# Performance work log

Hardware: AMD Instinct MI355X
Metric: run time of the kernel (lower is better)

Reference implementation:

```python
import jax, jax.numpy as jnp
import numpy as np

NUM_NODES = 2048
NUM_OPS = 8
D, F, K = 64, 64, 64
H_NG = 128
H_EE = 64


def _make_edges(n):
    # edges[0]=i (src), edges[1]=j (dst) for i in [2,n), j in [0,i)
    src = np.concatenate([np.full(i, i, dtype=np.int64) for i in range(2, n)])
    dst = np.concatenate([np.arange(i, dtype=np.int64) for i in range(2, n)])
    return np.stack([src, dst])


def setup_inputs() -> dict:
    key = jax.random.key(0)
    ks = jax.random.split(key, 8)
    n = NUM_NODES
    s = lambda k, shape, fan_in: jax.random.normal(k, shape, jnp.float32) * (1.0 / np.sqrt(fan_in))
    return {
        "embed": jax.random.normal(ks[0], (n, D), jnp.float32),
        "W1": s(ks[1], (D, H_NG), D), "b1": jnp.zeros((H_NG,), jnp.float32),
        "W2": s(ks[2], (H_NG, H_NG), H_NG), "b2": jnp.zeros((H_NG,), jnp.float32),
        "W3": s(ks[3], (H_NG, F), H_NG), "b3": jnp.zeros((F,), jnp.float32),
        "We1": s(ks[4], (2 * F, H_EE), 2 * F), "be1": jnp.zeros((H_EE,), jnp.float32),
        "We2": s(ks[5], (H_EE, K), H_EE), "be2": jnp.zeros((K,), jnp.float32),
        "Wop": s(ks[6], (K, NUM_OPS), K), "bop": jnp.zeros((NUM_OPS,), jnp.float32),
        "edges": jnp.asarray(_make_edges(n)),
        "weights": jnp.ones((_make_edges(n).shape[1],), jnp.float32),
    }


def gcn_conv(x, W, b, src, dst, ew, n):
    # PyG GCNConv: x' = D^{-1/2} (A + I) D^{-1/2} (x W) + b, aggregated at dst
    h = x @ W
    loop = jnp.arange(n)
    src2 = jnp.concatenate([src, loop])
    dst2 = jnp.concatenate([dst, loop])
    w2 = jnp.concatenate([ew, jnp.ones((n,), x.dtype)])
    deg = jax.ops.segment_sum(w2, dst2, num_segments=n)
    dinv = jnp.where(deg > 0, jax.lax.rsqrt(deg), 0.0)
    norm = dinv[src2] * w2 * dinv[dst2]
    out = jax.ops.segment_sum(h[src2] * norm[:, None], dst2, num_segments=n)
    return out + b


def reference(embed, W1, b1, W2, b2, W3, b3, We1, be1, We2, be2, Wop, bop, edges, weights):
    n = embed.shape[0]
    src, dst = edges[0], edges[1]
    h = jax.nn.relu(gcn_conv(embed, W1, b1, src, dst, weights, n))
    h = jax.nn.relu(gcn_conv(h, W2, b2, src, dst, weights, n))
    h = jax.nn.relu(gcn_conv(h, W3, b3, src, dst, weights, n))  # [n, F]
    e = jnp.concatenate([h[src], h[dst]], axis=-1)              # [E, 2F]
    e = jax.nn.relu(e @ We1 + be1)
    e = jax.nn.relu(e @ We2 + be2)
    o = e @ Wop + bop                                            # [E, num_ops]
    p = jax.nn.softmax(o, axis=-1)
    # forward loop skips i == num_nodes-1; those rows of p remain zero
    mask = (src < n - 1)[:, None]
    return jnp.where(mask, p, 0.0)
```

## Files before the change

### kernel.cpp

```cpp
#include <hip/hip_runtime.h>
#include <math.h>

#define NN 2048
#define LASTN 2047

typedef __attribute__((ext_vector_type(8))) short short8;
typedef __attribute__((ext_vector_type(4))) float f32x4;

__device__ __forceinline__ float node_dinv(int j) {
  int deg = (j < 2) ? 2047 : (2048 - j);
  return rsqrtf((float)deg);
}

__device__ __forceinline__ void split_bf(float x, short& h, short& l) {
  unsigned u = __float_as_uint(x);
  unsigned r = u + 0x7FFFu + ((u >> 16) & 1u);
  h = (short)(r >> 16);
  float fh = __uint_as_float((r >> 16) << 16);
  float res = x - fh;
  unsigned u2 = __float_as_uint(res);
  unsigned r2 = u2 + 0x7FFFu + ((u2 >> 16) & 1u);
  l = (short)(r2 >> 16);
}

__global__ __launch_bounds__(256) void gemm_node(const float* __restrict__ X,
                                                 const float* __restrict__ W,
                                                 const float* __restrict__ bias,
                                                 float* __restrict__ C, int K, int N) {
  int idx = blockIdx.x * 256 + threadIdx.x;
  int r = idx / N;
  int c = idx - r * N;
  float a0 = 0.f, a1 = 0.f, a2 = 0.f, a3 = 0.f;
  for (int k = 0; k < K; k += 4) {
    a0 = fmaf(X[r * K + k + 0], W[(k + 0) * N + c], a0);
    a1 = fmaf(X[r * K + k + 1], W[(k + 1) * N + c], a1);
    a2 = fmaf(X[r * K + k + 2], W[(k + 2) * N + c], a2);
    a3 = fmaf(X[r * K + k + 3], W[(k + 3) * N + c], a3);
  }
  C[idx] = (a0 + a1) + (a2 + a3) + (bias ? bias[c] : 0.f);
}

__global__ __launch_bounds__(256) void gemm_ab(const float* __restrict__ X,
                                               const float* __restrict__ We1,
                                               const float* __restrict__ be1,
                                               float* __restrict__ A,
                                               float* __restrict__ B) {
  int idx = blockIdx.x * 256 + threadIdx.x;
  int r = idx >> 6, c = idx & 63;
  const float* WA = We1;
  const float* WB = We1 + 64 * 64;
  float a0 = 0.f, a1 = 0.f, b0 = 0.f, b1 = 0.f;
  for (int k = 0; k < 64; k += 2) {
    float x0 = X[r * 64 + k], x1 = X[r * 64 + k + 1];
    a0 = fmaf(x0, WA[k * 64 + c], a0);
    a1 = fmaf(x1, WA[(k + 1) * 64 + c], a1);
    b0 = fmaf(x0, WB[k * 64 + c], b0);
    b1 = fmaf(x1, WB[(k + 1) * 64 + c], b1);
  }
  A[idx] = a0 + a1 + be1[c];
  B[idx] = b0 + b1;
}

__global__ __launch_bounds__(256) void gcn_agg(const float* __restrict__ H,
                                               const float* __restrict__ b,
                                               float* __restrict__ out, int N) {
  const int c = blockIdx.x;
  const int t = threadIdx.x;
  __shared__ float part[256];
  float s[8], hv[8];
  #pragma unroll
  for (int k = 0; k < 8; ++k) {
    int i = t * 8 + k;
    hv[k] = H[(size_t)i * N + c];
    s[k] = hv[k] * node_dinv(i);
  }
  float p = 0.f;
  #pragma unroll
  for (int k = 0; k < 8; ++k) p += s[k];
  part[t] = p;
  __syncthreads();
  for (int off = 1; off < 256; off <<= 1) {
    float v = part[t] + ((t + off < 256) ? part[t + off] : 0.f);
    __syncthreads();
    part[t] = v;
    __syncthreads();
  }
  float Q = (t < 255) ? part[t + 1] : 0.f;
  float Te[8];
  float acc = Q;
  #pragma unroll
  for (int k = 7; k >= 0; --k) { Te[k] = acc; acc += s[k]; }
  const float bc = b[c];
  #pragma unroll
  for (int k = 0; k < 8; ++k) {
    int j = t * 8 + k;
    float aggv = (j == 0) ? Te[1] : Te[k];
    float dj = node_dinv(j);
    float v = dj * aggv + hv[k] * dj * dj + bc;
    out[(size_t)j * N + c] = fmaxf(v, 0.f);
  }
}

__global__ __launch_bounds__(256) void prep_bfrag(const float* __restrict__ We2,
                                                  short* __restrict__ BfH,
                                                  short* __restrict__ BfL) {
  int t = blockIdx.x * 256 + threadIdx.x;
  if (t >= 512) return;
  int lane = t & 63;
  int rest = t >> 6;
  int ks = rest & 1;
  int ct = rest >> 1;
  int q = lane >> 4, l4 = lane & 15;
  int f = ct * 16 + l4;
  #pragma unroll
  for (int j = 0; j < 8; ++j) {
    int k = ks * 32 + q * 8 + j;
    float w = We2[k * 64 + f];
    short h, l;
    split_bf(w, h, l);
    int o = ((ct * 2 + ks) * 64 + lane) * 8 + j;
    BfH[o] = h;
    BfL[o] = l;
  }
}

#define CHUNK 192
#define LSTR 196

__global__ __launch_bounds__(256, 3) void edge_mlp(const float* __restrict__ Amat,
                                                   const float* __restrict__ Bmat,
                                                   const short* __restrict__ BfH,
                                                   const short* __restrict__ BfL,
                                                   const float* __restrict__ be2,
                                                   const float* __restrict__ Wop,
                                                   const float* __restrict__ bop,
                                                   float* __restrict__ out) {
  const int i = LASTN - blockIdx.x;
  const long base = (long)i * (i - 1) / 2 - 1;
  const int tid = threadIdx.x;

  if (i == LASTN) {
    const float4 z = make_float4(0.f, 0.f, 0.f, 0.f);
    for (int j = blockIdx.y * 256 + tid; j < LASTN; j += gridDim.y * 256) {
      size_t off = ((size_t)(base + j)) * 8;
      *(float4*)(out + off) = z;
      *(float4*)(out + off + 4) = z;
    }
    return;
  }

  __shared__ __align__(16) float sm[64 * LSTR];

  const int l = tid & 63, w = tid >> 6;
  const int l4 = l & 15, q = l >> 4;

  const float4* Arow = (const float4*)(Amat + (size_t)i * 64);
  const float4 a00 = Arow[q * 2], a01 = Arow[q * 2 + 1];
  const float4 a10 = Arow[8 + q * 2], a11 = Arow[8 + q * 2 + 1];

  short8 Bh[8], Bl[8];
  #pragma unroll
  for (int u = 0; u < 8; ++u) {
    Bh[u] = *(const short8*)(BfH + (u * 64 + l) * 8);
    Bl[u] = *(const short8*)(BfL + (u * 64 + l) * 8);
  }

  #pragma unroll 1
  for (int cidx = blockIdx.y; cidx * CHUNK < i; cidx += gridDim.y) {
    const int j0 = cidx * CHUNK;

    #pragma unroll 1
    for (int mt = 0; mt < 3; ++mt) {
      const int mbase = (w * 3 + mt) * 16;
      int j = j0 + mbase + l4;
      int jc = min(j, i - 1);
      const float4* Brow = (const float4*)(Bmat + (size_t)jc * 64);

      short8 ah[2], al[2];
      #pragma unroll
      for (int ks = 0; ks < 2; ++ks) {
        float4 bb0 = Brow[ks * 8 + q * 2];
        float4 bb1 = Brow[ks * 8 + q * 2 + 1];
        float4 aa0 = ks ? a10 : a00;
        float4 aa1 = ks ? a11 : a01;
        float v0 = fmaxf(aa0.x + bb0.x, 0.f), v1 = fmaxf(aa0.y + bb0.y, 0.f);
        float v2 = fmaxf(aa0.z + bb0.z, 0.f), v3 = fmaxf(aa0.w + bb0.w, 0.f);
        float v4 = fmaxf(aa1.x + bb1.x, 0.f), v5 = fmaxf(aa1.y + bb1.y, 0.f);
        float v6 = fmaxf(aa1.z + bb1.z, 0.f), v7 = fmaxf(aa1.w + bb1.w, 0.f);
        short h0, h1, h2, h3, h4, h5, h6, h7, L0, L1, L2, L3, L4, L5, L6, L7;
        split_bf(v0, h0, L0); split_bf(v1, h1, L1);
        split_bf(v2, h2, L2); split_bf(v3, h3, L3);
        split_bf(v4, h4, L4); split_bf(v5, h5, L5);
        split_bf(v6, h6, L6); split_bf(v7, h7, L7);
        ah[ks] = (short8){h0, h1, h2, h3, h4, h5, h6, h7};
        al[ks] = (short8){L0, L1, L2, L3, L4, L5, L6, L7};
      }

      f32x4 acc[4];
      #pragma unroll
      for (int ct = 0; ct < 4; ++ct) acc[ct] = (f32x4){0.f, 0.f, 0.f, 0.f};
      #pragma unroll
      for (int ct = 0; ct < 4; ++ct)
        acc[ct] = __builtin_amdgcn_mfma_f32_16x16x32_bf16(ah[0], Bh[ct * 2 + 0], acc[ct], 0, 0, 0);
      #pragma unroll
      for (int ct = 0; ct < 4; ++ct)
        acc[ct] = __builtin_amdgcn_mfma_f32_16x16x32_bf16(ah[1], Bh[ct * 2 + 1], acc[ct], 0, 0, 0);
      #pragma unroll
      for (int ct = 0; ct < 4; ++ct)
        acc[ct] = __builtin_amdgcn_mfma_f32_16x16x32_bf16(ah[0], Bl[ct * 2 + 0], acc[ct], 0, 0, 0);
      #pragma unroll
      for (int ct = 0; ct < 4; ++ct)
        acc[ct] = __builtin_amdgcn_mfma_f32_16x16x32_bf16(ah[1], Bl[ct * 2 + 1], acc[ct], 0, 0, 0);
      #pragma unroll
      for (int ct = 0; ct < 4; ++ct)
        acc[ct] = __builtin_amdgcn_mfma_f32_16x16x32_bf16(al[0], Bh[ct * 2 + 0], acc[ct], 0, 0, 0);
      #pragma unroll
      for (int ct = 0; ct < 4; ++ct)
        acc[ct] = __builtin_amdgcn_mfma_f32_16x16x32_bf16(al[1], Bh[ct * 2 + 1], acc[ct], 0, 0, 0);

      #pragma unroll
      for (int ct = 0; ct < 4; ++ct) {
        int f = ct * 16 + l4;
        float bias = be2[f];
        float4 st;
        st.x = fmaxf(acc[ct][0] + bias, 0.f);
        st.y = fmaxf(acc[ct][1] + bias, 0.f);
        st.z = fmaxf(acc[ct][2] + bias, 0.f);
        st.w = fmaxf(acc[ct][3] + bias, 0.f);
        *(float4*)(&sm[f * LSTR + mbase + q * 4]) = st;
      }
    }
    __syncthreads();

    if (tid < CHUNK) {
      int j = j0 + tid;
      if (j < i) {
        float o0 = bop[0], o1 = bop[1], o2 = bop[2], o3 = bop[3];
        float o4 = bop[4], o5 = bop[5], o6 = bop[6], o7 = bop[7];
        #pragma unroll 8
        for (int f = 0; f < 64; ++f) {
          float v = sm[f * LSTR + tid];
          o0 = fmaf(v, Wop[f * 8 + 0], o0);
          o1 = fmaf(v, Wop[f * 8 + 1], o1);
          o2 = fmaf(v, Wop[f * 8 + 2], o2);
          o3 = fmaf(v, Wop[f * 8 + 3], o3);
          o4 = fmaf(v, Wop[f * 8 + 4], o4);
          o5 = fmaf(v, Wop[f * 8 + 5], o5);
          o6 = fmaf(v, Wop[f * 8 + 6], o6);
          o7 = fmaf(v, Wop[f * 8 + 7], o7);
        }
        float mx = fmaxf(fmaxf(fmaxf(o0, o1), fmaxf(o2, o3)),
                         fmaxf(fmaxf(o4, o5), fmaxf(o6, o7)));
        float p0 = __expf(o0 - mx), p1 = __expf(o1 - mx), p2 = __expf(o2 - mx);
        float p3 = __expf(o3 - mx), p4 = __expf(o4 - mx), p5 = __expf(o5 - mx);
        float p6 = __expf(o6 - mx), p7 = __expf(o7 - mx);
        float rs = 1.0f / (((p0 + p1) + (p2 + p3)) + ((p4 + p5) + (p6 + p7)));
        size_t off = ((size_t)(base + j)) * 8;
        *(float4*)(out + off) = make_float4(p0 * rs, p1 * rs, p2 * rs, p3 * rs);
        *(float4*)(out + off + 4) = make_float4(p4 * rs, p5 * rs, p6 * rs, p7 * rs);
      }
    }
    __syncthreads();
  }
}

extern "C" void kernel_launch(void* const* d_in, const int* in_sizes, int n_in,
                              void* d_out, int out_size, void* d_ws, size_t ws_size,
                              hipStream_t stream) {
  const float* embed = (const float*)d_in[0];
  const float* W1 = (const float*)d_in[1];
  const float* b1 = (const float*)d_in[2];
  const float* W2 = (const float*)d_in[3];
  const float* b2 = (const float*)d_in[4];
  const float* W3 = (const float*)d_in[5];
  const float* b3 = (const float*)d_in[6];
  const float* We1 = (const float*)d_in[7];
  const float* be1 = (const float*)d_in[8];
  const float* We2 = (const float*)d_in[9];
  const float* be2 = (const float*)d_in[10];
  const float* Wop = (const float*)d_in[11];
  const float* bop = (const float*)d_in[12];

  float* ws = (float*)d_ws;
  float* Hbuf = ws;
  float* hbuf = ws + 262144;
  float* Abuf = ws + 524288;
  float* Bbuf = ws + 655360;
  short* BfH = (short*)(ws + 786432);
  short* BfL = (short*)(ws + 786432 + 2048);
  float* outp = (float*)d_out;

  prep_bfrag<<<2, 256, 0, stream>>>(We2, BfH, BfL);

  gemm_node<<<(2048 * 128) / 256, 256, 0, stream>>>(embed, W1, nullptr, Hbuf, 64, 128);
  gcn_agg<<<128, 256, 0, stream>>>(Hbuf, b1, hbuf, 128);
  gemm_node<<<(2048 * 128) / 256, 256, 0, stream>>>(hbuf, W2, nullptr, Hbuf, 128, 128);
  gcn_agg<<<128, 256, 0, stream>>>(Hbuf, b2, hbuf, 128);
  gemm_node<<<(2048 * 64) / 256, 256, 0, stream>>>(hbuf, W3, nullptr, Hbuf, 128, 64);
  gcn_agg<<<64, 256, 0, stream>>>(Hbuf, b3, hbuf, 64);
  gemm_ab<<<(2048 * 64) / 256, 256, 0, stream>>>(hbuf, We1, be1, Abuf, Bbuf);

  dim3 ge(2046, 4, 1);
  edge_mlp<<<ge, 256, 0, stream>>>(Abuf, Bbuf, BfH, BfL, be2, Wop, bop, outp);
}
```

Measured before the change: 291.2 us.

## Fuse GCN gemm and aggregation per column with transposed layout; packed bf16 split

Each GCN layer's node matmul is merged with its prefix-sum aggregation into one kernel per output column. Activations are kept in a transposed (feature-major) layout, and a prep kernel transposes the embedding alongside building the We2 fragments. This cuts the launch count from 8 to 5 and removes the intermediate H round trip. The edge MLP's hi/lo bf16 split now uses the packed v_cvt_pk_bf16_f32 instruction to reduce the instruction count in the hot loop. Risks are low parallelism in the fused layer kernel (only 64-128 blocks) and possible rounding differences from the hardware conversion.

After: 266.8 us. 1.09x faster.

```diff
diff --git a/kernel.cpp b/kernel.cpp
--- a/kernel.cpp
+++ b/kernel.cpp
@@ -6,6 +6,7 @@
 
 typedef __attribute__((ext_vector_type(8))) short short8;
 typedef __attribute__((ext_vector_type(4))) float f32x4;
+typedef __attribute__((ext_vector_type(4))) unsigned uint4v;
 
 __device__ __forceinline__ float node_dinv(int j) {
   int deg = (j < 2) ? 2047 : (2048 - j);
@@ -23,24 +24,117 @@
   l = (short)(r2 >> 16);
 }
 
-__global__ __launch_bounds__(256) void gemm_node(const float* __restrict__ X,
-                                                 const float* __restrict__ W,
-                                                 const float* __restrict__ bias,
-                                                 float* __restrict__ C, int K, int N) {
-  int idx = blockIdx.x * 256 + threadIdx.x;
-  int r = idx / N;
-  int c = idx - r * N;
+__device__ __forceinline__ unsigned cvt_pk_bf16(float a, float b) {
+  unsigned r;
+  asm("v_cvt_pk_bf16_f32 %0, %1, %2" : "=v"(r) : "v"(a), "v"(b));
+  return r;
+}
+
+__device__ __forceinline__ void split_pair(float a, float b, unsigned& h, unsigned& l) {
+  h = cvt_pk_bf16(a, b);
+  float fa = __uint_as_float(h << 16);
+  float fb = __uint_as_float(h & 0xFFFF0000u);
+  l = cvt_pk_bf16(a - fa, b - fb);
+}
+
+__global__ __launch_bounds__(256) void prep(const float* __restrict__ embed,
+                                            const float* __restrict__ We2,
+                                            float* __restrict__ embedT,
+                                            short* __restrict__ BfH,
+                                            short* __restrict__ BfL) {
+  __shared__ float tile[64][65];
+  const int b = blockIdx.x;
+  const int t = threadIdx.x;
+  if (b < 32) {
+    #pragma unroll
+    for (int m = 0; m < 16; ++m) {
+      int idx = m * 256 + t;
+      int rl = idx >> 6, cc = idx & 63;
+      tile[rl][cc] = embed[(b * 64 + rl) * 64 + cc];
+    }
+    __syncthreads();
+    #pragma unroll
+    for (int m = 0; m < 16; ++m) {
+      int idx = m * 256 + t;
+      int cc = idx >> 6, rl = idx & 63;
+      embedT[cc * 2048 + b * 64 + rl] = tile[rl][cc];
+    }
+  } else {
+    int tt = (b - 32) * 256 + t;
+    int lane = tt & 63;
+    int rest = tt >> 6;
+    int ks = rest & 1;
+    int ct = rest >> 1;
+    int q = lane >> 4, l4 = lane & 15;
+    int f = ct * 16 + l4;
+    #pragma unroll
+    for (int j = 0; j < 8; ++j) {
+      int k = ks * 32 + q * 8 + j;
+      float w = We2[k * 64 + f];
+      short h, l;
+      split_bf(w, h, l);
+      int o = ((ct * 2 + ks) * 64 + lane) * 8 + j;
+      BfH[o] = h;
+      BfL[o] = l;
+    }
+  }
+}
+
+template <int K>
+__global__ __launch_bounds__(512) void layer_fused(const float* __restrict__ XT,
+                                                   const float* __restrict__ W,
+                                                   const float* __restrict__ bias,
+                                                   float* __restrict__ outT, int N) {
+  const int c = blockIdx.x;
+  const int t = threadIdx.x;
+  __shared__ float wcol[K];
+  __shared__ float sm[2048];
+  __shared__ float part[512];
+  if (t < K) wcol[t] = W[t * N + c];
+  __syncthreads();
   float a0 = 0.f, a1 = 0.f, a2 = 0.f, a3 = 0.f;
-  for (int k = 0; k < K; k += 4) {
-    a0 = fmaf(X[r * K + k + 0], W[(k + 0) * N + c], a0);
-    a1 = fmaf(X[r * K + k + 1], W[(k + 1) * N + c], a1);
-    a2 = fmaf(X[r * K + k + 2], W[(k + 2) * N + c], a2);
-    a3 = fmaf(X[r * K + k + 3], W[(k + 3) * N + c], a3);
-  }
-  C[idx] = (a0 + a1) + (a2 + a3) + (bias ? bias[c] : 0.f);
-}
-
-__global__ __launch_bounds__(256) void gemm_ab(const float* __restrict__ X,
+  #pragma unroll 8
+  for (int k = 0; k < K; ++k) {
+    const float wk = wcol[k];
+    const float* xr = XT + k * 2048 + t;
+    a0 = fmaf(xr[0], wk, a0);
+    a1 = fmaf(xr[512], wk, a1);
+    a2 = fmaf(xr[1024], wk, a2);
+    a3 = fmaf(xr[1536], wk, a3);
+  }
+  sm[t] = a0 * node_dinv(t);
+  sm[t + 512] = a1 * node_dinv(t + 512);
+  sm[t + 1024] = a2 * node_dinv(t + 1024);
+  sm[t + 1536] = a3 * node_dinv(t + 1536);
+  __syncthreads();
+  const int j0 = 4 * t;
+  float s0 = sm[j0], s1 = sm[j0 + 1], s2 = sm[j0 + 2], s3 = sm[j0 + 3];
+  part[t] = (s0 + s1) + (s2 + s3);
+  __syncthreads();
+  for (int off = 1; off < 512; off <<= 1) {
+    float v = part[t] + ((t + off < 512) ? part[t + off] : 0.f);
+    __syncthreads();
+    part[t] = v;
+    __syncthreads();
+  }
+  float Q = (t < 511) ? part[t + 1] : 0.f;
+  float Te3 = Q;
+  float Te2 = Te3 + s3;
+  float Te1 = Te2 + s2;
+  float Te0 = Te1 + s1;
+  const float bc = bias[c];
+  float g0 = (j0 == 0) ? Te1 : Te0;
+  float d0 = node_dinv(j0), d1 = node_dinv(j0 + 1);
+  float d2 = node_dinv(j0 + 2), d3 = node_dinv(j0 + 3);
+  float4 o;
+  o.x = fmaxf(d0 * g0 + s0 * d0 + bc, 0.f);
+  o.y = fmaxf(d1 * Te1 + s1 * d1 + bc, 0.f);
+  o.z = fmaxf(d2 * Te2 + s2 * d2 + bc, 0.f);
+  o.w = fmaxf(d3 * Te3 + s3 * d3 + bc, 0.f);
+  *(float4*)(outT + (size_t)c * 2048 + j0) = o;
+}
+
+__global__ __launch_bounds__(256) void gemm_ab(const float* __restrict__ XT,
                                                const float* __restrict__ We1,
                                                const float* __restrict__ be1,
                                                float* __restrict__ A,
@@ -51,7 +145,7 @@
   const float* WB = We1 + 64 * 64;
   float a0 = 0.f, a1 = 0.f, b0 = 0.f, b1 = 0.f;
   for (int k = 0; k < 64; k += 2) {
-    float x0 = X[r * 64 + k], x1 = X[r * 64 + k + 1];
+    float x0 = XT[k * 2048 + r], x1 = XT[(k + 1) * 2048 + r];
     a0 = fmaf(x0, WA[k * 64 + c], a0);
     a1 = fmaf(x1, WA[(k + 1) * 64 + c], a1);
     b0 = fmaf(x0, WB[k * 64 + c], b0);
@@ -59,69 +153,6 @@
   }
   A[idx] = a0 + a1 + be1[c];
   B[idx] = b0 + b1;
-}
-
-__global__ __launch_bounds__(256) void gcn_agg(const float* __restrict__ H,
-                                               const float* __restrict__ b,
-                                               float* __restrict__ out, int N) {
-  const int c = blockIdx.x;
-  const int t = threadIdx.x;
-  __shared__ float part[256];
-  float s[8], hv[8];
-  #pragma unroll
-  for (int k = 0; k < 8; ++k) {
-    int i = t * 8 + k;
-    hv[k] = H[(size_t)i * N + c];
-    s[k] = hv[k] * node_dinv(i);
-  }
-  float p = 0.f;
-  #pragma unroll
-  for (int k = 0; k < 8; ++k) p += s[k];
-  part[t] = p;
-  __syncthreads();
-  for (int off = 1; off < 256; off <<= 1) {
-    float v = part[t] + ((t + off < 256) ? part[t + off] : 0.f);
-    __syncthreads();
-    part[t] = v;
-    __syncthreads();
-  }
-  float Q = (t < 255) ? part[t + 1] : 0.f;
-  float Te[8];
-  float acc = Q;
-  #pragma unroll
-  for (int k = 7; k >= 0; --k) { Te[k] = acc; acc += s[k]; }
-  const float bc = b[c];
-  #pragma unroll
-  for (int k = 0; k < 8; ++k) {
-    int j = t * 8 + k;
-    float aggv = (j == 0) ? Te[1] : Te[k];
-    float dj = node_dinv(j);
-    float v = dj * aggv + hv[k] * dj * dj + bc;
-    out[(size_t)j * N + c] = fmaxf(v, 0.f);
-  }
-}
-
-__global__ __launch_bounds__(256) void prep_bfrag(const float* __restrict__ We2,
-                                                  short* __restrict__ BfH,
-                                                  short* __restrict__ BfL) {
-  int t = blockIdx.x * 256 + threadIdx.x;
-  if (t >= 512) return;
-  int lane = t & 63;
-  int rest = t >> 6;
-  int ks = rest & 1;
-  int ct = rest >> 1;
-  int q = lane >> 4, l4 = lane & 15;
-  int f = ct * 16 + l4;
-  #pragma unroll
-  for (int j = 0; j < 8; ++j) {
-    int k = ks * 32 + q * 8 + j;
-    float w = We2[k * 64 + f];
-    short h, l;
-    split_bf(w, h, l);
-    int o = ((ct * 2 + ks) * 64 + lane) * 8 + j;
-    BfH[o] = h;
-    BfL[o] = l;
-  }
 }
 
 #define CHUNK 192
@@ -187,13 +218,13 @@
         float v2 = fmaxf(aa0.z + bb0.z, 0.f), v3 = fmaxf(aa0.w + bb0.w, 0.f);
         float v4 = fmaxf(aa1.x + bb1.x, 0.f), v5 = fmaxf(aa1.y + bb1.y, 0.f);
         float v6 = fmaxf(aa1.z + bb1.z, 0.f), v7 = fmaxf(aa1.w + bb1.w, 0.f);
-        short h0, h1, h2, h3, h4, h5, h6, h7, L0, L1, L2, L3, L4, L5, L6, L7;
-        split_bf(v0, h0, L0); split_bf(v1, h1, L1);
-        split_bf(v2, h2, L2); split_bf(v3, h3, L3);
-        split_bf(v4, h4, L4); split_bf(v5, h5, L5);
-        split_bf(v6, h6, L6); split_bf(v7, h7, L7);
-        ah[ks] = (short8){h0, h1, h2, h3, h4, h5, h6, h7};
-        al[ks] = (short8){L0, L1, L2, L3, L4, L5, L6, L7};
+        unsigned h0, h1, h2, h3, L0, L1, L2, L3;
+        split_pair(v0, v1, h0, L0);
+        split_pair(v2, v3, h1, L1);
+        split_pair(v4, v5, h2, L2);
+        split_pair(v6, v7, h3, L3);
+        ah[ks] = __builtin_bit_cast(short8, (uint4v){h0, h1, h2, h3});
+        al[ks] = __builtin_bit_cast(short8, (uint4v){L0, L1, L2, L3});
       }
 
       f32x4 acc[4];
@@ -282,23 +313,21 @@
   const float* bop = (const float*)d_in[12];
 
   float* ws = (float*)d_ws;
-  float* Hbuf = ws;
-  float* hbuf = ws + 262144;
-  float* Abuf = ws + 524288;
-  float* Bbuf = ws + 655360;
-  short* BfH = (short*)(ws + 786432);
-  short* BfL = (short*)(ws + 786432 + 2048);
+  float* embedT = ws;
+  float* h2T = ws;
+  float* h1T = ws + 262144;
+  float* Abuf = ws + 262144;
+  float* Bbuf = ws + 393216;
+  float* h3T = ws + 524288;
+  short* BfH = (short*)(ws + 655360);
+  short* BfL = (short*)(ws + 657408);
   float* outp = (float*)d_out;
 
-  prep_bfrag<<<2, 256, 0, stream>>>(We2, BfH, BfL);
-
-  gemm_node<<<(2048 * 128) / 256, 256, 0, stream>>>(embed, W1, nullptr, Hbuf, 64, 128);
-  gcn_agg<<<128, 256, 0, stream>>>(Hbuf, b1, hbuf, 128);
-  gemm_node<<<(2048 * 128) / 256, 256, 0, stream>>>(hbuf, W2, nullptr, Hbuf, 128, 128);
-  gcn_agg<<<128, 256, 0, stream>>>(Hbuf, b2, hbuf, 128);
-  gemm_node<<<(2048 * 64) / 256, 256, 0, stream>>>(hbuf, W3, nullptr, Hbuf, 128, 64);
-  gcn_agg<<<64, 256, 0, stream>>>(Hbuf, b3, hbuf, 64);
-  gemm_ab<<<(2048 * 64) / 256, 256, 0, stream>>>(hbuf, We1, be1, Abuf, Bbuf);
+  prep<<<34, 256, 0, stream>>>(embed, We2, embedT, BfH, BfL);
+  layer_fused<64><<<128, 512, 0, stream>>>(embedT, W1, b1, h1T, 128);
+  layer_fused<128><<<128, 512, 0, stream>>>(h1T, W2, b2, h2T, 128);
+  layer_fused<128><<<64, 512, 0, stream>>>(h2T, W3, b3, h3T, 64);
+  gemm_ab<<<512, 256, 0, stream>>>(h3T, We1, be1, Abuf, Bbuf);
 
   dim3 ge(2046, 4, 1);
   edge_mlp<<<ge, 256, 0, stream>>>(Abuf, Bbuf, BfH, BfL, be2, Wop, bop, outp);
```
